# Kernel optimization log

Hardware: AMD Instinct MI355X
Metric: run time of the kernel (lower is better)

The kernel has to match this reference:

```python
import jax, jax.numpy as jnp
import numpy as np
import math

B, FREQ, TIME, E = 4, 256, 512, 512

def _sinusoid_table(max_len, d_model):
    # Matches torch: pe[:,0::2]=sin(pos*div), pe[:,1::2]=cos(pos*div)
    pos = np.arange(max_len, dtype=np.float32)[:, None]
    div = np.exp(np.arange(0, d_model, 2, dtype=np.float32) * (-math.log(10000.0) / d_model))
    pe = np.zeros((max_len, d_model), dtype=np.float32)
    pe[:, 0::2] = np.sin(pos * div)
    pe[:, 1::2] = np.cos(pos * div)
    return jnp.asarray(pe)

def setup_inputs() -> dict:
    key = jax.random.key(0)
    x = jax.random.normal(key, (B, FREQ * TIME, E), dtype=jnp.float32)
    pe_1d = _sinusoid_table(max(FREQ, TIME), E)  # only rows actually used
    return {"x": x, "pe_1d": pe_1d, "freq_dim": FREQ, "time_dim": TIME}

def reference(x, pe_1d, freq_dim, time_dim):
    # Vectorized form of the original double loop: pe_2d[f*T+t] = pe_f[f] + pe_t[t]
    pe_f = pe_1d[:freq_dim]                      # [F, E]
    pe_t = pe_1d[:time_dim]                      # [T, E]
    pe_2d = (pe_f[:, None, :] + pe_t[None, :, :]).reshape(freq_dim * time_dim, -1)  # [F*T, E]
    # Dropout is identity in eval mode (deterministic reference)
    return x + pe_2d[None, :, :]
```

## Files before the change

kernel.cpp:

```cpp
#include <hip/hip_runtime.h>


typedef float f32x4 __attribute__((ext_vector_type(4)));

constexpr int  B_    = 4;
constexpr int  FREQ_ = 256;
constexpr int  TIME_ = 512;
constexpr int  E_    = 512;
constexpr int  E4    = E_ / 4;
constexpr int  ROWS  = FREQ_ * TIME_;
constexpr long N4T   = (long)B_ * ROWS * E4;

constexpr int BLOCK = 256;
constexpr int ITERS = 16;
constexpr int CHUNK = BLOCK * ITERS;
constexpr int GRID  = (int)(N4T / CHUNK);

static_assert(CHUNK % E4 == 0, "chunk row-aligned");
static_assert((CHUNK / E4) <= TIME_ && TIME_ % (CHUNK / E4) == 0, "f const per block");
static_assert(((long)ROWS * E4) % CHUNK == 0, "b const per block");

__global__ void __launch_bounds__(BLOCK)
pe2d_add_kernel(const f32x4* __restrict__ x,
                const f32x4* __restrict__ pe,
                f32x4* __restrict__ out)
{
    const int base    = blockIdx.x * CHUNK;
    const int tid     = threadIdx.x;
    const int e4      = tid & (E4 - 1);
    const int dt      = tid >> 7;
    const int rowbase = (base >> 7) & (ROWS - 1);
    const int f       = rowbase >> 9;
    const f32x4 pf    = pe[f * E4 + e4];

    int i = base + tid;
    int t = (rowbase & (TIME_ - 1)) + dt;

    #pragma unroll 8
    for (int it = 0; it < ITERS; ++it) {
        f32x4 v = __builtin_nontemporal_load(&x[i]);
        const f32x4 pt = pe[t * E4 + e4];
        v = v + pf + pt;
        __builtin_nontemporal_store(v, &out[i]);
        i += BLOCK;
        t += 2;
    }
}

extern "C" void kernel_launch(void* const* d_in, const int* in_sizes, int n_in,
                              void* d_out, int out_size, void* d_ws, size_t ws_size,
                              hipStream_t stream)
{
    const f32x4* x  = (const f32x4*)d_in[0];
    const f32x4* pe = (const f32x4*)d_in[1];
    f32x4* out = (f32x4*)d_out;

    pe2d_add_kernel<<<GRID, BLOCK, 0, stream>>>(x, pe, out);
}
```

Before: 393.4 us.

## Switch to grid-stride loop and derive frequency PE via angle-addition rotation

```diff
diff --git a/kernel.cpp b/kernel.cpp
--- a/kernel.cpp
+++ b/kernel.cpp
@@ -11,39 +11,53 @@
 constexpr int  ROWS  = FREQ_ * TIME_;
 constexpr long N4T   = (long)B_ * ROWS * E4;
 
-constexpr int BLOCK = 256;
-constexpr int ITERS = 16;
-constexpr int CHUNK = BLOCK * ITERS;
-constexpr int GRID  = (int)(N4T / CHUNK);
+constexpr int BLOCK    = 256;
+constexpr int GRID     = 16384;
+constexpr int NTHREADS = GRID * BLOCK;
+constexpr int STRIDE   = NTHREADS;
+constexpr int ITERS    = (int)(N4T / NTHREADS);
+constexpr int ROWSTEP  = STRIDE / E4;
+constexpr int ITERS_PER_BATCH = ROWS / ROWSTEP;
+constexpr int FSTEP    = ROWSTEP / TIME_;
 
-static_assert(CHUNK % E4 == 0, "chunk row-aligned");
-static_assert((CHUNK / E4) <= TIME_ && TIME_ % (CHUNK / E4) == 0, "f const per block");
-static_assert(((long)ROWS * E4) % CHUNK == 0, "b const per block");
+static_assert(ROWSTEP % TIME_ == 0, "t invariant per thread");
+static_assert(ROWS % ROWSTEP == 0, "batch boundary aligns with iterations");
+static_assert(ITERS == B_ * ITERS_PER_BATCH, "iter count");
 
 __global__ void __launch_bounds__(BLOCK)
 pe2d_add_kernel(const f32x4* __restrict__ x,
                 const f32x4* __restrict__ pe,
                 f32x4* __restrict__ out)
 {
-    const int base    = blockIdx.x * CHUNK;
-    const int tid     = threadIdx.x;
-    const int e4      = tid & (E4 - 1);
-    const int dt      = tid >> 7;
-    const int rowbase = (base >> 7) & (ROWS - 1);
-    const int f       = rowbase >> 9;
-    const f32x4 pf    = pe[f * E4 + e4];
+    const int i0  = blockIdx.x * BLOCK + threadIdx.x;
+    const int e4  = i0 & (E4 - 1);
+    const int row = i0 >> 7;
+    const int t   = row & (TIME_ - 1);
+    const int f0  = row >> 9;
 
-    int i = base + tid;
-    int t = (rowbase & (TIME_ - 1)) + dt;
+    const f32x4 pt  = pe[t     * E4 + e4];
+    const f32x4 pf0 = pe[f0    * E4 + e4];
+    const f32x4 rot = pe[FSTEP * E4 + e4];
 
-    #pragma unroll 8
-    for (int it = 0; it < ITERS; ++it) {
-        f32x4 v = __builtin_nontemporal_load(&x[i]);
-        const f32x4 pt = pe[t * E4 + e4];
-        v = v + pf + pt;
-        __builtin_nontemporal_store(v, &out[i]);
-        i += BLOCK;
-        t += 2;
+    int i = i0;
+
+    #pragma unroll
+    for (int b = 0; b < B_; ++b) {
+        f32x4 pf = pf0;
+        #pragma unroll
+        for (int k = 0; k < ITERS_PER_BATCH; ++k) {
+            f32x4 v = __builtin_nontemporal_load(&x[i]);
+            v = v + pf + pt;
+            __builtin_nontemporal_store(v, &out[i]);
+            i += STRIDE;
+
+            f32x4 np;
+            np.x = pf.x * rot.y + pf.y * rot.x;
+            np.y = pf.y * rot.y - pf.x * rot.x;
+            np.z = pf.z * rot.w + pf.w * rot.z;
+            np.w = pf.w * rot.w - pf.z * rot.z;
+            pf = np;
+        }
     }
 }
 
```

Measured after the change: 384.0 us (median of 2 runs). 2.4% less time.
